# Kernel tuning notes

Measured on AMD Instinct MI355X. Metric: run time of the kernel, lower is better.

## Reference

```python
import jax, jax.numpy as jnp
import numpy as np

# dims
B, N, D, H, L = 2, 4096, 768, 12, 2
DH = D // H          # 64, equals BigBird block_size
BS = 64              # block size
NB = N // BS         # 64 blocks
R = 3                # num_random_blocks
FF = 4 * D
EPS = 1e-12          # BigBird layer_norm_eps


def _ln(x, g, b):
    mu = jnp.mean(x, -1, keepdims=True)
    var = jnp.mean(jnp.square(x - mu), -1, keepdims=True)
    return (x - mu) * jax.lax.rsqrt(var + EPS) * g + b


def _gelu_new(x):
    c = np.sqrt(2.0 / np.pi).astype(np.float32)
    return 0.5 * x * (1.0 + jnp.tanh(c * (x + 0.044715 * x * x * x)))


def _block_sparse_attn(q, k, v, rb):
    # q,k,v: [B,H,N,DH]; rb: [H,NB,R] random block ids (constant)
    scale = 1.0 / np.sqrt(DH).astype(np.float32)
    qb = q.reshape(B, H, NB, BS, DH)
    kb = k.reshape(B, H, NB, BS, DH)
    vb = v.reshape(B, H, NB, BS, DH)
    M = NB - 2
    mids = jnp.arange(1, NB - 1)
    win = jnp.stack([mids - 1, mids, mids + 1], -1)                    # [M,3]
    glb = jnp.broadcast_to(jnp.array([0, NB - 1], jnp.int32), (M, 2))  # [M,2]
    idx = jnp.concatenate([
        jnp.broadcast_to(glb[None], (H, M, 2)),
        jnp.broadcast_to(win[None], (H, M, 3)),
        rb[:, 1:NB - 1, :]], axis=-1)                                  # [H,M,8]
    hh = jnp.arange(H)[:, None, None]
    # gather key/value blocks: [B,H,M,8,BS,DH] -> [B,H,M,512,DH]
    kg = kb[:, hh, idx].reshape(B, H, M, -1, DH)
    vg = vb[:, hh, idx].reshape(B, H, M, -1, DH)
    qm = qb[:, :, 1:NB - 1]                                            # [B,H,M,BS,DH]
    s = jnp.einsum('bhmqd,bhmkd->bhmqk', qm, kg) * scale
    cm = jnp.einsum('bhmqk,bhmkd->bhmqd', jax.nn.softmax(s, -1), vg)
    # first and last query blocks attend globally (full attention)
    qe = jnp.stack([qb[:, :, 0], qb[:, :, -1]], 2)                     # [B,H,2,BS,DH]
    se = jnp.einsum('bheqd,bhkd->bheqk', qe, k) * scale
    ce = jnp.einsum('bheqk,bhkd->bheqd', jax.nn.softmax(se, -1), v)
    out = jnp.concatenate([ce[:, :, :1], cm, ce[:, :, 1:]], axis=2)    # [B,H,NB,BS,DH]
    return out.reshape(B, H, N, DH)


def _forward(inputs_embeds, rand_blocks, pos_emb, tt_emb, emb_ln_g, emb_ln_b,
             Wq, bq, Wk, bk, Wv, bv, Wo, bo, ln1_g, ln1_b,
             Wi, bi, Wd, bd, ln2_g, ln2_b, fc_w, fc_b):
    x = inputs_embeds + pos_emb[None] + tt_emb                         # embeddings (token_type id 0)
    x = _ln(x, emb_ln_g, emb_ln_b)
    for l in range(L):
        q = (x @ Wq[l] + bq[l]).reshape(B, N, H, DH).transpose(0, 2, 1, 3)
        k = (x @ Wk[l] + bk[l]).reshape(B, N, H, DH).transpose(0, 2, 1, 3)
        v = (x @ Wv[l] + bv[l]).reshape(B, N, H, DH).transpose(0, 2, 1, 3)
        ctx = _block_sparse_attn(q, k, v, rand_blocks[l])
        ctx = ctx.transpose(0, 2, 1, 3).reshape(B, N, D)
        a = _ln(x + ctx @ Wo[l] + bo[l], ln1_g[l], ln1_b[l])
        h = _gelu_new(a @ Wi[l] + bi[l])
        x = _ln(a + h @ Wd[l] + bd[l], ln2_g[l], ln2_b[l])
    pooled = jnp.mean(x, axis=1)                                       # [B,D]; dropout is identity at eval
    return (pooled @ fc_w + fc_b).squeeze()                            # [B]


def setup_inputs() -> dict:
    key = jax.random.key(0)
    ks = jax.random.split(key, 24)
    s = 0.02
    nrm = lambda k, shp: jax.random.normal(k, shp, jnp.float32) * s
    return {
        'inputs_embeds': jax.random.normal(ks[0], (B, N, D), jnp.float32),
        'rand_blocks': jax.random.randint(ks[1], (L, H, NB, R), 0, NB, jnp.int32),
        'pos_emb': nrm(ks[2], (N, D)),
        'tt_emb': nrm(ks[3], (D,)),
        'emb_ln_g': jnp.ones((D,), jnp.float32), 'emb_ln_b': jnp.zeros((D,), jnp.float32),
        'Wq': nrm(ks[4], (L, D, D)), 'bq': jnp.zeros((L, D), jnp.float32),
        'Wk': nrm(ks[5], (L, D, D)), 'bk': jnp.zeros((L, D), jnp.float32),
        'Wv': nrm(ks[6], (L, D, D)), 'bv': jnp.zeros((L, D), jnp.float32),
        'Wo': nrm(ks[7], (L, D, D)), 'bo': jnp.zeros((L, D), jnp.float32),
        'ln1_g': jnp.ones((L, D), jnp.float32), 'ln1_b': jnp.zeros((L, D), jnp.float32),
        'Wi': nrm(ks[8], (L, D, FF)), 'bi': jnp.zeros((L, FF), jnp.float32),
        'Wd': nrm(ks[9], (L, FF, D)), 'bd': jnp.zeros((L, D), jnp.float32),
        'ln2_g': jnp.ones((L, D), jnp.float32), 'ln2_b': jnp.zeros((L, D), jnp.float32),
        'fc_w': nrm(ks[10], (D, 1)), 'fc_b': jnp.zeros((1,), jnp.float32),
    }


def reference(inputs_embeds, rand_blocks, pos_emb, tt_emb, emb_ln_g, emb_ln_b,
              Wq, bq, Wk, bk, Wv, bv, Wo, bo, ln1_g, ln1_b,
              Wi, bi, Wd, bd, ln2_g, ln2_b, fc_w, fc_b):
    return _forward(inputs_embeds, rand_blocks, pos_emb, tt_emb, emb_ln_g, emb_ln_b,
                    Wq, bq, Wk, bk, Wv, bv, Wo, bo, ln1_g, ln1_b,
                    Wi, bi, Wd, bd, ln2_g, ln2_b, fc_w, fc_b)
```

## Files before the change

### kernel.cpp

```cpp
#include <hip/hip_runtime.h>
#include <math.h>

#define B_ 2
#define N_ 4096
#define D_ 768
#define H_ 12
#define DH_ 64
#define NB_ 64
#define FF_ 3072
#define LAYERS_ 2
#define ROWS_ (B_ * N_)

typedef __attribute__((ext_vector_type(8))) short s16x8;
typedef __attribute__((ext_vector_type(8))) unsigned short u16x8;
typedef __attribute__((ext_vector_type(4))) float f32x4;

typedef const __attribute__((address_space(1))) unsigned int ga_u32;
typedef __attribute__((address_space(3))) unsigned int lds_u32;

static __device__ __forceinline__ float gelu_fast(float x) {
    float z2 = 1.5957691216057308f * x * (1.0f + 0.044715f * x * x);
    return x * __builtin_amdgcn_rcpf(1.0f + __expf(-z2));
}

static __device__ __forceinline__ unsigned bf16_rne(float f) {
    unsigned u = __float_as_uint(f);
    return (u + 0x7FFFu + ((u >> 16) & 1u)) >> 16;
}
static __device__ __forceinline__ float bfh2f(unsigned short h) {
    return __uint_as_float(((unsigned)h) << 16);
}

__global__ __launch_bounds__(256)
void prep_weights(const float* __restrict__ Wq, const float* __restrict__ Wk,
                  const float* __restrict__ Wv, const float* __restrict__ Wo,
                  const float* __restrict__ Wi, const float* __restrict__ Wd,
                  unsigned short* __restrict__ Wt) {
    const size_t LW = 7077888;
    int bid = blockIdx.x;
    int l = bid / 1728, r = bid % 1728;
    const float* W; unsigned short* T; int K, N, t, nx;
    if (r < 576) {
        int which = r / 144; t = r % 144; nx = 12; K = 768; N = 768;
        W = (which == 0 ? Wq : which == 1 ? Wk : which == 2 ? Wv : Wo) + (size_t)l * D_ * D_;
        T = Wt + l * LW + (size_t)(which < 3 ? which * 768 * 768 : 2304 * 768);
    } else if (r < 1152) {
        t = r - 576; nx = 48; K = 768; N = 3072;
        W = Wi + (size_t)l * D_ * FF_;
        T = Wt + l * LW + (size_t)(2304 * 768 + 768 * 768);
    } else {
        t = r - 1152; nx = 12; K = 3072; N = 768;
        W = Wd + (size_t)l * FF_ * D_;
        T = Wt + l * LW + (size_t)(2304 * 768 + 768 * 768 + 3072 * 768);
    }
    const int bx = t % nx, by = t / nx;
    __shared__ unsigned short tile[64][72];
    const int k0 = by * 64, n0 = bx * 64;
    const int tt = threadIdx.x;
    const int rr = tt >> 2, c0 = (tt & 3) * 16;
    const float* src = W + (size_t)(k0 + rr) * N + n0 + c0;
#pragma unroll
    for (int j = 0; j < 4; ++j) {
        float4 v = *(const float4*)(src + j * 4);
        tile[rr][c0 + j * 4 + 0] = (unsigned short)bf16_rne(v.x);
        tile[rr][c0 + j * 4 + 1] = (unsigned short)bf16_rne(v.y);
        tile[rr][c0 + j * 4 + 2] = (unsigned short)bf16_rne(v.z);
        tile[rr][c0 + j * 4 + 3] = (unsigned short)bf16_rne(v.w);
    }
    __syncthreads();
    const int nr = tt >> 2, kc = (tt & 3) * 16;
    unsigned short* dst = T + (size_t)(n0 + nr) * K + k0 + kc;
    ushort4 o;
#pragma unroll
    for (int j = 0; j < 4; ++j) {
        o.x = tile[kc + j * 4 + 0][nr];
        o.y = tile[kc + j * 4 + 1][nr];
        o.z = tile[kc + j * 4 + 2][nr];
        o.w = tile[kc + j * 4 + 3][nr];
        *(ushort4*)(dst + j * 4) = o;
    }
}

template <int OMODE>
__global__ __launch_bounds__(256)
void gemm_bt(const unsigned short* __restrict__ A, const unsigned short* __restrict__ Bt,
             const float* __restrict__ bias, void* __restrict__ Cv,
             int N, int K, int gelu) {
    __shared__ __align__(16) unsigned short smem[2 * 8192];
    const int tid = threadIdx.x, lane = tid & 63, wid = tid >> 6;
    const int bid = blockIdx.x;
    const int row0 = (bid & 63) * 128, col0 = (bid >> 6) * 128;
    const int rh = (wid >> 1) * 64, ch = (wid & 1) * 64;
    const int fr = lane & 15, fq = lane >> 4;
    const int srow = wid * 32 + (lane >> 2);
    const int skoff = (lane & 3) * 8;
    const unsigned short* gA0 = A + (size_t)(row0 + srow) * K + skoff;
    const unsigned short* gA1 = gA0 + (size_t)16 * K;
    const unsigned short* gB0 = Bt + (size_t)(col0 + srow) * K + skoff;
    const unsigned short* gB1 = gB0 + (size_t)16 * K;

    f32x4 acc[4][4] = {};
    const int nk = K >> 5;
    {
        unsigned short* s = smem;
        __builtin_amdgcn_global_load_lds((ga_u32*)gA0, (lds_u32*)&s[wid * 1024], 16, 0, 0);
        __builtin_amdgcn_global_load_lds((ga_u32*)gA1, (lds_u32*)&s[wid * 1024 + 512], 16, 0, 0);
        __builtin_amdgcn_global_load_lds((ga_u32*)gB0, (lds_u32*)&s[4096 + wid * 1024], 16, 0, 0);
        __builtin_amdgcn_global_load_lds((ga_u32*)gB1, (lds_u32*)&s[4096 + wid * 1024 + 512], 16, 0, 0);
    }
    for (int kt = 0; kt < nk; ++kt) {
        __syncthreads();
        if (kt + 1 < nk) {
            int k0 = (kt + 1) << 5;
            unsigned short* s = smem + ((kt + 1) & 1) * 8192;
            __builtin_amdgcn_global_load_lds((ga_u32*)(gA0 + k0), (lds_u32*)&s[wid * 1024], 16, 0, 0);
            __builtin_amdgcn_global_load_lds((ga_u32*)(gA1 + k0), (lds_u32*)&s[wid * 1024 + 512], 16, 0, 0);
            __builtin_amdgcn_global_load_lds((ga_u32*)(gB0 + k0), (lds_u32*)&s[4096 + wid * 1024], 16, 0, 0);
            __builtin_amdgcn_global_load_lds((ga_u32*)(gB1 + k0), (lds_u32*)&s[4096 + wid * 1024 + 512], 16, 0, 0);
        }
        const unsigned short* sA = smem + (kt & 1) * 8192;
        const unsigned short* sB = sA + 4096;
        s16x8 af[4], bf[4];
#pragma unroll
        for (int i = 0; i < 4; ++i)
            af[i] = *(const s16x8*)&sA[(rh + 16 * i + fr) * 32 + fq * 8];
#pragma unroll
        for (int j = 0; j < 4; ++j)
            bf[j] = *(const s16x8*)&sB[(ch + 16 * j + fr) * 32 + fq * 8];
#pragma unroll
        for (int i = 0; i < 4; ++i)
#pragma unroll
            for (int j = 0; j < 4; ++j)
                acc[i][j] = __builtin_amdgcn_mfma_f32_16x16x32_bf16(af[i], bf[j], acc[i][j], 0, 0, 0);
    }
    if (OMODE == 0) {
#pragma unroll
        for (int j = 0; j < 4; ++j) {
            int col = col0 + ch + 16 * j + fr;
            float bb = bias[col];
#pragma unroll
            for (int i = 0; i < 4; ++i)
#pragma unroll
                for (int r = 0; r < 4; ++r) {
                    int row = row0 + rh + 16 * i + fq * 4 + r;
                    float v = acc[i][j][r] + bb;
                    if (gelu) v = gelu_fast(v);
                    ((float*)Cv)[(size_t)row * N + col] = v;
                }
        }
    } else {
        unsigned short* sC = smem;
#pragma unroll
        for (int hh = 0; hh < 2; ++hh) {
            __syncthreads();
            if ((wid >> 1) == hh) {
#pragma unroll
                for (int j = 0; j < 4; ++j) {
                    float bb = bias[col0 + ch + 16 * j + fr];
#pragma unroll
                    for (int i = 0; i < 4; ++i)
#pragma unroll
                        for (int r = 0; r < 4; ++r) {
                            float v = acc[i][j][r] + bb;
                            if (gelu) v = gelu_fast(v);
                            sC[(16 * i + fq * 4 + r) * 136 + ch + 16 * j + fr] =
                                (unsigned short)bf16_rne(v);
                        }
                }
            }
            __syncthreads();
#pragma unroll
            for (int p = 0; p < 4; ++p) {
                int seg = p * 256 + tid;
                int r = seg >> 4, c8 = (seg & 15) * 8;
                *(u16x8*)&((unsigned short*)Cv)[(size_t)(row0 + hh * 64 + r) * N + col0 + c8] =
                    *(const u16x8*)&sC[r * 136 + c8];
            }
        }
    }
}

__global__ __launch_bounds__(256)
void gemm_qkv(const unsigned short* __restrict__ A, const unsigned short* __restrict__ Bt,
              const float* __restrict__ bq, const float* __restrict__ bk,
              const float* __restrict__ bv,
              unsigned short* __restrict__ Qh, unsigned short* __restrict__ Kh,
              unsigned short* __restrict__ VT) {
    const int K = D_;
    __shared__ __align__(16) unsigned short smem[2 * 8192];
    const int tid = threadIdx.x, lane = tid & 63, wid = tid >> 6;
    const int bid = blockIdx.x;
    const int row0 = (bid & 63) * 128;
    const int bx = bid >> 6;
    const int col0 = bx * 128;
    const int rh = (wid >> 1) * 64, ch = (wid & 1) * 64;
    const int fr = lane & 15, fq = lane >> 4;
    const int srow = wid * 32 + (lane >> 2);
    const int skoff = (lane & 3) * 8;
    const unsigned short* gA0 = A + (size_t)(row0 + srow) * K + skoff;
    const unsigned short* gA1 = gA0 + (size_t)16 * K;
    const unsigned short* gB0 = Bt + (size_t)(col0 + srow) * K + skoff;
    const unsigned short* gB1 = gB0 + (size_t)16 * K;

    f32x4 acc[4][4] = {};
    const int nk = K >> 5;
    {
        unsigned short* s = smem;
        __builtin_amdgcn_global_load_lds((ga_u32*)gA0, (lds_u32*)&s[wid * 1024], 16, 0, 0);
        __builtin_amdgcn_global_load_lds((ga_u32*)gA1, (lds_u32*)&s[wid * 1024 + 512], 16, 0, 0);
        __builtin_amdgcn_global_load_lds((ga_u32*)gB0, (lds_u32*)&s[4096 + wid * 1024], 16, 0, 0);
        __builtin_amdgcn_global_load_lds((ga_u32*)gB1, (lds_u32*)&s[4096 + wid * 1024 + 512], 16, 0, 0);
    }
    for (int kt = 0; kt < nk; ++kt) {
        __syncthreads();
        if (kt + 1 < nk) {
            int k0 = (kt + 1) << 5;
            unsigned short* s = smem + ((kt + 1) & 1) * 8192;
            __builtin_amdgcn_global_load_lds((ga_u32*)(gA0 + k0), (lds_u32*)&s[wid * 1024], 16, 0, 0);
            __builtin_amdgcn_global_load_lds((ga_u32*)(gA1 + k0), (lds_u32*)&s[wid * 1024 + 512], 16, 0, 0);
            __builtin_amdgcn_global_load_lds((ga_u32*)(gB0 + k0), (lds_u32*)&s[4096 + wid * 1024], 16, 0, 0);
            __builtin_amdgcn_global_load_lds((ga_u32*)(gB1 + k0), (lds_u32*)&s[4096 + wid * 1024 + 512], 16, 0, 0);
        }
        const unsigned short* sA = smem + (kt & 1) * 8192;
        const unsigned short* sB = sA + 4096;
        s16x8 af[4], bf[4];
#pragma unroll
        for (int i = 0; i < 4; ++i)
            af[i] = *(const s16x8*)&sA[(rh + 16 * i + fr) * 32 + fq * 8];
#pragma unroll
        for (int j = 0; j < 4; ++j)
            bf[j] = *(const s16x8*)&sB[(ch + 16 * j + fr) * 32 + fq * 8];
#pragma unroll
        for (int i = 0; i < 4; ++i)
#pragma unroll
            for (int j = 0; j < 4; ++j)
                acc[i][j] = __builtin_amdgcn_mfma_f32_16x16x32_bf16(af[i], bf[j], acc[i][j], 0, 0, 0);
    }
    const int seg = bx / 6;
    const int colbase = col0 - seg * D_;
    const float* bias = (seg == 0) ? bq : (seg == 1) ? bk : bv;
    if (seg == 2) {
#pragma unroll
        for (int j = 0; j < 4; ++j) {
            int col_l = colbase + ch + 16 * j + fr;
            float bb = bias[col_l];
#pragma unroll
            for (int i = 0; i < 4; ++i) {
                int rowbase = row0 + rh + 16 * i + fq * 4;
                ushort4 o;
                o.x = (unsigned short)bf16_rne(acc[i][j][0] + bb);
                o.y = (unsigned short)bf16_rne(acc[i][j][1] + bb);
                o.z = (unsigned short)bf16_rne(acc[i][j][2] + bb);
                o.w = (unsigned short)bf16_rne(acc[i][j][3] + bb);
                *(ushort4*)&VT[(size_t)col_l * ROWS_ + rowbase] = o;
            }
        }
    } else {
        unsigned short* dst = (seg == 0) ? Qh : Kh;
        unsigned short* sC = smem;
#pragma unroll
        for (int hh = 0; hh < 2; ++hh) {
            __syncthreads();
            if ((wid >> 1) == hh) {
#pragma unroll
                for (int j = 0; j < 4; ++j) {
                    float bb = bias[colbase + ch + 16 * j + fr];
#pragma unroll
                    for (int i = 0; i < 4; ++i)
#pragma unroll
                        for (int r = 0; r < 4; ++r)
                            sC[(16 * i + fq * 4 + r) * 136 + ch + 16 * j + fr] =
                                (unsigned short)bf16_rne(acc[i][j][r] + bb);
                }
            }
            __syncthreads();
#pragma unroll
            for (int p = 0; p < 4; ++p) {
                int seg2 = p * 256 + tid;
                int r = seg2 >> 4, c8 = (seg2 & 15) * 8;
                *(u16x8*)&dst[(size_t)(row0 + hh * 64 + r) * D_ + colbase + c8] =
                    *(const u16x8*)&sC[r * 136 + c8];
            }
        }
    }
}

template <bool EDGE>
__global__ __launch_bounds__(256, 4)
void attn_mfma(const unsigned short* __restrict__ Qb, const unsigned short* __restrict__ Kb,
               const unsigned short* __restrict__ VTb, const int* __restrict__ rb,
               unsigned short* __restrict__ ctx, float* __restrict__ scratch) {
    __shared__ __align__(16) unsigned short sQ[64][72];
    __shared__ __align__(16) unsigned short sK[64][72];
    __shared__ __align__(16) unsigned short sVT[64][72];
    __shared__ __align__(16) unsigned short sP[4][16][72];
    __shared__ int sList[16];
    const int tid = threadIdx.x, lane = tid & 63, wid = tid >> 6;
    const int fr = lane & 15, fq = lane >> 4;
    int qb, h, b, nkb, slice = 0;
    if (EDGE) {
        int part = blockIdx.x & 3;
        int hh = (blockIdx.x >> 2) % H_;
        int be = (blockIdx.x >> 2) / H_;
        int eb = be & 1;
        b = be >> 1;
        h = hh;
        qb = eb ? (NB_ - 1) : 0;
        nkb = 16;
        slice = ((b * 2 + eb) * H_ + h) * 4 + part;
        if (tid < 16) sList[tid] = part * 16 + tid;
    } else {
        qb = blockIdx.x % (NB_ - 2) + 1;
        h = (blockIdx.x / (NB_ - 2)) % H_;
        b = blockIdx.x / ((NB_ - 2) * H_);
        nkb = 8;
        if (tid < 8) {
            int e;
            if (tid == 0) e = 0;
            else if (tid == 1) e = NB_ - 1;
            else if (tid < 5) e = qb + (tid - 3);
            else e = rb[(h * NB_ + qb) * 3 + (tid - 5)];
            sList[tid] = e;
        }
    }
    const int qrow0 = b * N_ + qb * 64;
    const unsigned short* Qg = Qb + (size_t)qrow0 * D_ + h * 64;
#pragma unroll
    for (int p = 0; p < 2; ++p) {
        int idx = p * 256 + tid;
        int r = idx >> 3, o = (idx & 7) * 8;
        *(u16x8*)&sQ[r][o] = *(const u16x8*)(Qg + (size_t)r * D_ + o);
    }
    f32x4 oacc[4] = {};
    float l_part[4] = {};
    __syncthreads();
    s16x8 aq0 = *(const s16x8*)&sQ[wid * 16 + fr][fq * 8];
    s16x8 aq1 = *(const s16x8*)&sQ[wid * 16 + fr][32 + fq * 8];

    const int stg_r = tid >> 3, stg_o = (tid & 7) * 8;
    u16x8 kreg[2], vreg[2];
    {
        int keyrow0 = b * N_ + sList[0] * 64;
        const unsigned short* Kg = Kb + (size_t)keyrow0 * D_ + h * 64;
        const unsigned short* Vg = VTb + (size_t)(h * 64) * ROWS_ + keyrow0;
#pragma unroll
        for (int p = 0; p < 2; ++p) {
            int r = stg_r + p * 32;
            kreg[p] = *(const u16x8*)(Kg + (size_t)r * D_ + stg_o);
            vreg[p] = *(const u16x8*)(Vg + (size_t)r * ROWS_ + stg_o);
        }
    }

    for (int kb = 0; kb < nkb; ++kb) {
        __syncthreads();
#pragma unroll
        for (int p = 0; p < 2; ++p) {
            int r = stg_r + p * 32;
            *(u16x8*)&sK[r][stg_o] = kreg[p];
            *(u16x8*)&sVT[r][stg_o] = vreg[p];
        }
        __syncthreads();
        if (kb + 1 < nkb) {
            int keyrow0 = b * N_ + sList[kb + 1] * 64;
            const unsigned short* Kg = Kb + (size_t)keyrow0 * D_ + h * 64;
            const unsigned short* Vg = VTb + (size_t)(h * 64) * ROWS_ + keyrow0;
#pragma unroll
            for (int p = 0; p < 2; ++p) {
                int r = stg_r + p * 32;
                kreg[p] = *(const u16x8*)(Kg + (size_t)r * D_ + stg_o);
                vreg[p] = *(const u16x8*)(Vg + (size_t)r * ROWS_ + stg_o);
            }
        }
#pragma unroll
        for (int g = 0; g < 4; ++g) {
            s16x8 bk0 = *(const s16x8*)&sK[g * 16 + fr][fq * 8];
            s16x8 bk1 = *(const s16x8*)&sK[g * 16 + fr][32 + fq * 8];
            f32x4 s = {};
            s = __builtin_amdgcn_mfma_f32_16x16x32_bf16(aq0, bk0, s, 0, 0, 0);
            s = __builtin_amdgcn_mfma_f32_16x16x32_bf16(aq1, bk1, s, 0, 0, 0);
#pragma unroll
            for (int r = 0; r < 4; ++r) {
                float pv = __expf(s[r] * 0.125f);
                l_part[r] += pv;
                sP[wid][fq * 4 + r][g * 16 + fr] = (unsigned short)bf16_rne(pv);
            }
        }
        s16x8 ap0 = *(const s16x8*)&sP[wid][fr][fq * 8];
        s16x8 ap1 = *(const s16x8*)&sP[wid][fr][32 + fq * 8];
#pragma unroll
        for (int g = 0; g < 4; ++g) {
            s16x8 bv0 = *(const s16x8*)&sVT[g * 16 + fr][fq * 8];
            s16x8 bv1 = *(const s16x8*)&sVT[g * 16 + fr][32 + fq * 8];
            oacc[g] = __builtin_amdgcn_mfma_f32_16x16x32_bf16(ap0, bv0, oacc[g], 0, 0, 0);
            oacc[g] = __builtin_amdgcn_mfma_f32_16x16x32_bf16(ap1, bv1, oacc[g], 0, 0, 0);
        }
    }
    float l4[4];
#pragma unroll
    for (int r = 0; r < 4; ++r) {
        float lv = l_part[r];
        lv += __shfl_xor(lv, 1, 64);
        lv += __shfl_xor(lv, 2, 64);
        lv += __shfl_xor(lv, 4, 64);
        lv += __shfl_xor(lv, 8, 64);
        l4[r] = lv;
    }
    if (EDGE) {
        float* sc = scratch + (size_t)slice * (64 * 64 + 64);
#pragma unroll
        for (int g = 0; g < 4; ++g)
#pragma unroll
            for (int r = 0; r < 4; ++r)
                sc[(wid * 16 + fq * 4 + r) * 64 + g * 16 + fr] = oacc[g][r];
        if (fr == 0) {
#pragma unroll
            for (int r = 0; r < 4; ++r)
                sc[4096 + wid * 16 + fq * 4 + r] = l4[r];
        }
    } else {
        __syncthreads();
#pragma unroll
        for (int g = 0; g < 4; ++g) {
#pragma unroll
            for (int r = 0; r < 4; ++r) {
                float v = oacc[g][r] / l4[r];
                sK[wid * 16 + fq * 4 + r][g * 16 + fr] = (unsigned short)bf16_rne(v);
            }
        }
        __syncthreads();
        unsigned short* Cg = ctx + (size_t)qrow0 * D_ + h * 64;
#pragma unroll
        for (int p = 0; p < 2; ++p) {
            int idx = p * 256 + tid;
            int r = idx >> 3, o = (idx & 7) * 8;
            *(u16x8*)(Cg + (size_t)r * D_ + o) = *(const u16x8*)&sK[r][o];
        }
    }
}

__global__ __launch_bounds__(256)
void edge_combine(const float* __restrict__ scratch, unsigned short* __restrict__ ctx) {
    const int bid = blockIdx.x;
    const int h = bid % H_;
    const int eb = (bid / H_) & 1;
    const int b = bid / (2 * H_);
    const int qb = eb ? (NB_ - 1) : 0;
    const int qrow0 = b * N_ + qb * 64;
    const int slice0 = bid * 4;
    for (int e = threadIdx.x; e < 4096; e += 256) {
        int row = e >> 6, col = e & 63;
        float o = 0.f, l = 0.f;
#pragma unroll
        for (int p = 0; p < 4; ++p) {
            const float* sc = scratch + (size_t)(slice0 + p) * (64 * 64 + 64);
            o += sc[row * 64 + col];
            l += sc[4096 + row];
        }
        ctx[(size_t)(qrow0 + row) * D_ + h * 64 + col] = (unsigned short)bf16_rne(o / l);
    }
}

__global__ __launch_bounds__(256)
void embed_ln_kernel(const float* __restrict__ emb, const float* __restrict__ pos,
                     const float* __restrict__ tt, const float* __restrict__ g,
                     const float* __restrict__ bb, unsigned short* __restrict__ out) {
    __shared__ float red1[4], red2[4];
    const int row = blockIdx.x;
    const int n = row & (N_ - 1);
    const int t = threadIdx.x;
    float v[3];
#pragma unroll
    for (int i = 0; i < 3; ++i) {
        int d = t + i * 256;
        v[i] = emb[(size_t)row * D_ + d] + pos[(size_t)n * D_ + d] + tt[d];
    }
    float s = v[0] + v[1] + v[2];
#pragma unroll
    for (int off = 32; off > 0; off >>= 1) s += __shfl_xor(s, off, 64);
    if ((t & 63) == 0) red1[t >> 6] = s;
    __syncthreads();
    float mu = (red1[0] + red1[1] + red1[2] + red1[3]) * (1.0f / D_);
    float q = 0;
#pragma unroll
    for (int i = 0; i < 3; ++i) { float dv = v[i] - mu; q += dv * dv; }
#pragma unroll
    for (int off = 32; off > 0; off >>= 1) q += __shfl_xor(q, off, 64);
    if ((t & 63) == 0) red2[t >> 6] = q;
    __syncthreads();
    float var = (red2[0] + red2[1] + red2[2] + red2[3]) * (1.0f / D_);
    float rs = rsqrtf(var + 1e-12f);
#pragma unroll
    for (int i = 0; i < 3; ++i) {
        int d = t + i * 256;
        out[(size_t)row * D_ + d] = (unsigned short)bf16_rne((v[i] - mu) * rs * g[d] + bb[d]);
    }
}

__global__ __launch_bounds__(256)
void add_ln_kernel(const unsigned short* __restrict__ X, const unsigned short* __restrict__ Y,
                   const float* __restrict__ g, const float* __restrict__ bb,
                   unsigned short* __restrict__ out) {
    __shared__ float red1[4], red2[4];
    const int row = blockIdx.x;
    const int t = threadIdx.x;
    float v[3];
#pragma unroll
    for (int i = 0; i < 3; ++i) {
        int d = t + i * 256;
        v[i] = bfh2f(X[(size_t)row * D_ + d]) + bfh2f(Y[(size_t)row * D_ + d]);
    }
    float s = v[0] + v[1] + v[2];
#pragma unroll
    for (int off = 32; off > 0; off >>= 1) s += __shfl_xor(s, off, 64);
    if ((t & 63) == 0) red1[t >> 6] = s;
    __syncthreads();
    float mu = (red1[0] + red1[1] + red1[2] + red1[3]) * (1.0f / D_);
    float q = 0;
#pragma unroll
    for (int i = 0; i < 3; ++i) { float dv = v[i] - mu; q += dv * dv; }
#pragma unroll
    for (int off = 32; off > 0; off >>= 1) q += __shfl_xor(q, off, 64);
    if ((t & 63) == 0) red2[t >> 6] = q;
    __syncthreads();
    float var = (red2[0] + red2[1] + red2[2] + red2[3]) * (1.0f / D_);
    float rs = rsqrtf(var + 1e-12f);
#pragma unroll
    for (int i = 0; i < 3; ++i) {
        int d = t + i * 256;
        out[(size_t)row * D_ + d] = (unsigned short)bf16_rne((v[i] - mu) * rs * g[d] + bb[d]);
    }
}

__global__ __launch_bounds__(256)
void pool_partial_kernel(const unsigned short* __restrict__ X, float* __restrict__ partial) {
    int blk = blockIdx.x;
    int b = blk >> 4, c = blk & 15;
    int t = threadIdx.x;
#pragma unroll
    for (int i = 0; i < 3; ++i) {
        int d = t + i * 256;
        float s = 0.f;
        for (int n = 0; n < 256; ++n)
            s += bfh2f(X[((size_t)(b * N_ + c * 256 + n)) * D_ + d]);
        partial[(size_t)(b * 16 + c) * D_ + d] = s;
    }
}

__global__ __launch_bounds__(256)
void pool_final_kernel(const float* __restrict__ partial, const float* __restrict__ fcw,
                       const float* __restrict__ fcb, float* __restrict__ out) {
    __shared__ float red[4];
    int t = threadIdx.x;
    for (int b = 0; b < B_; ++b) {
        float s = 0.f;
#pragma unroll
        for (int i = 0; i < 3; ++i) {
            int d = t + i * 256;
            float ps = 0.f;
#pragma unroll
            for (int c = 0; c < 16; ++c) ps += partial[(size_t)(b * 16 + c) * D_ + d];
            s += ps * (1.0f / N_) * fcw[d];
        }
#pragma unroll
        for (int off = 32; off > 0; off >>= 1) s += __shfl_xor(s, off, 64);
        __syncthreads();
        if ((t & 63) == 0) red[t >> 6] = s;
        __syncthreads();
        if (t == 0) out[b] = red[0] + red[1] + red[2] + red[3] + fcb[0];
    }
}

extern "C" void kernel_launch(void* const* d_in, const int* in_sizes, int n_in,
                              void* d_out, int out_size, void* d_ws, size_t ws_size,
                              hipStream_t stream) {
    (void)in_sizes; (void)n_in; (void)out_size; (void)ws_size;
    const float* emb  = (const float*)d_in[0];
    const int*   rblk = (const int*)d_in[1];
    const float* pos  = (const float*)d_in[2];
    const float* tt   = (const float*)d_in[3];
    const float* elg  = (const float*)d_in[4];
    const float* elb  = (const float*)d_in[5];
    const float* Wq   = (const float*)d_in[6];
    const float* bq   = (const float*)d_in[7];
    const float* Wk   = (const float*)d_in[8];
    const float* bk   = (const float*)d_in[9];
    const float* Wv   = (const float*)d_in[10];
    const float* bv   = (const float*)d_in[11];
    const float* Wo   = (const float*)d_in[12];
    const float* bo   = (const float*)d_in[13];
    const float* ln1g = (const float*)d_in[14];
    const float* ln1b = (const float*)d_in[15];
    const float* Wi   = (const float*)d_in[16];
    const float* bi   = (const float*)d_in[17];
    const float* Wd   = (const float*)d_in[18];
    const float* bd   = (const float*)d_in[19];
    const float* ln2g = (const float*)d_in[20];
    const float* ln2b = (const float*)d_in[21];
    const float* fcw  = (const float*)d_in[22];
    const float* fcb  = (const float*)d_in[23];
    float* outp = (float*)d_out;

    const size_t R = (size_t)ROWS_ * D_;
    float* base = (float*)d_ws;
    unsigned short* Xh  = (unsigned short*)base;
    unsigned short* Abh = (unsigned short*)(base + R / 2);
    unsigned short* Ob  = (unsigned short*)(base + R);
    unsigned short* Qh  = (unsigned short*)(base + 2 * R);
    unsigned short* Kh  = (unsigned short*)(base + 2 * R + R / 2);
    unsigned short* VTh = (unsigned short*)(base + 3 * R);
    unsigned short* Ch  = (unsigned short*)(base + 3 * R + R / 2);
    unsigned short* Hh  = (unsigned short*)(base + 2 * R);
    unsigned short* Wt  = (unsigned short*)(base + 4 * R);
    float* Esc = base + 4 * R + 7077888;
    float* Pp  = Esc + 798720;

    const size_t LW = 7077888;
    const int rows = ROWS_;
    dim3 blk(256);

    prep_weights<<<2 * 1728, blk, 0, stream>>>(Wq, Wk, Wv, Wo, Wi, Wd, Wt);

    embed_ln_kernel<<<rows, blk, 0, stream>>>(emb, pos, tt, elg, elb, Xh);

    for (int l = 0; l < LAYERS_; ++l) {
        const float* bq_l = bq + (size_t)l * D_;
        const float* bk_l = bk + (size_t)l * D_;
        const float* bv_l = bv + (size_t)l * D_;
        const float* bo_l = bo + (size_t)l * D_;
        const float* bi_l = bi + (size_t)l * FF_;
        const float* bd_l = bd + (size_t)l * D_;
        const float* l1g = ln1g + (size_t)l * D_;
        const float* l1b = ln1b + (size_t)l * D_;
        const float* l2g = ln2g + (size_t)l * D_;
        const float* l2b = ln2b + (size_t)l * D_;
        const int* rb_l = rblk + (size_t)l * H_ * NB_ * 3;
        unsigned short* QKVt = Wt + l * LW;
        unsigned short* Ot = QKVt + 2304 * 768;
        unsigned short* It = Ot + 768 * 768;
        unsigned short* Dt = It + 3072 * 768;

        gemm_qkv<<<18 * 64, blk, 0, stream>>>(Xh, QKVt, bq_l, bk_l, bv_l, Qh, Kh, VTh);

        attn_mfma<false><<<B_ * H_ * (NB_ - 2), blk, 0, stream>>>(Qh, Kh, VTh, rb_l, Ch, Esc);
        attn_mfma<true><<<B_ * 2 * H_ * 4, blk, 0, stream>>>(Qh, Kh, VTh, rb_l, Ch, Esc);
        edge_combine<<<B_ * 2 * H_, blk, 0, stream>>>(Esc, Ch);

        gemm_bt<1><<<6 * 64, blk, 0, stream>>>(Ch, Ot, bo_l, Ob, D_, D_, 0);
        add_ln_kernel<<<rows, blk, 0, stream>>>(Xh, Ob, l1g, l1b, Abh);

        gemm_bt<1><<<24 * 64, blk, 0, stream>>>(Abh, It, bi_l, Hh, FF_, D_, 1);
        gemm_bt<1><<<6 * 64, blk, 0, stream>>>(Hh, Dt, bd_l, Ob, D_, FF_, 0);

        add_ln_kernel<<<rows, blk, 0, stream>>>(Abh, Ob, l2g, l2b, Xh);
    }

    pool_partial_kernel<<<B_ * 16, blk, 0, stream>>>(Xh, Pp);
    pool_final_kernel<<<1, blk, 0, stream>>>(Pp, fcw, fcb, outp);
}
```

Baseline: 747.7 us.

## Use 256x128 GEMM tiles for QKV/FFN-up and split-K for FFN-down

Adds 256x128-tile GEMM kernels (8x4 MFMA accumulators per wave, two blocks per CU) for the QKV projection and the FFN up-projection, which halves the number of blocks and raises operand reuse per LDS load. The FFN down-projection (K=3072, only 384 tiles) is split into two K halves via blockIdx.y, each writing bf16 partial sums, and a new add_ln2 kernel sums the residual with both partials before the layer norm. This targets CU under-utilisation on the narrow down-projection GEMM. The cost is extra partial-sum traffic, a bf16 rounding of each partial, and higher register pressure in the larger tiles.

```diff
diff --git a/kernel.cpp b/kernel.cpp
--- a/kernel.cpp
+++ b/kernel.cpp
@@ -81,26 +81,240 @@
     }
 }
 
-template <int OMODE>
+__global__ __launch_bounds__(256, 2)
+void gemm_bt256(const unsigned short* __restrict__ A, const unsigned short* __restrict__ Bt,
+                const float* __restrict__ bias, unsigned short* __restrict__ Cv,
+                int N, int K, int gelu) {
+    __shared__ __align__(16) unsigned short smem[2 * 12288];
+    const int tid = threadIdx.x, lane = tid & 63, wid = tid >> 6;
+    const int bid = blockIdx.x;
+    const int row0 = (bid & 31) * 256, col0 = (bid >> 5) * 128;
+    const int wh = wid >> 1, wc = wid & 1;
+    const int fr = lane & 15, fq = lane >> 4;
+    const int slr = lane >> 2, slo = (lane & 3) * 8;
+
+    const unsigned short* gA[4];
+    const unsigned short* gB[2];
+#pragma unroll
+    for (int c = 0; c < 4; ++c)
+        gA[c] = A + (size_t)(row0 + wid * 64 + c * 16 + slr) * K + slo;
+#pragma unroll
+    for (int c = 0; c < 2; ++c)
+        gB[c] = Bt + (size_t)(col0 + wid * 32 + c * 16 + slr) * K + slo;
+
+    f32x4 acc[8][4] = {};
+    const int nk = K >> 5;
+    {
+        unsigned short* s = smem;
+#pragma unroll
+        for (int c = 0; c < 4; ++c)
+            __builtin_amdgcn_global_load_lds((ga_u32*)gA[c],
+                (lds_u32*)&s[(wid * 64 + c * 16) * 32], 16, 0, 0);
+#pragma unroll
+        for (int c = 0; c < 2; ++c)
+            __builtin_amdgcn_global_load_lds((ga_u32*)gB[c],
+                (lds_u32*)&s[8192 + (wid * 32 + c * 16) * 32], 16, 0, 0);
+    }
+    for (int kt = 0; kt < nk; ++kt) {
+        __syncthreads();
+        if (kt + 1 < nk) {
+            int k0 = (kt + 1) << 5;
+            unsigned short* s = smem + ((kt + 1) & 1) * 12288;
+#pragma unroll
+            for (int c = 0; c < 4; ++c)
+                __builtin_amdgcn_global_load_lds((ga_u32*)(gA[c] + k0),
+                    (lds_u32*)&s[(wid * 64 + c * 16) * 32], 16, 0, 0);
+#pragma unroll
+            for (int c = 0; c < 2; ++c)
+                __builtin_amdgcn_global_load_lds((ga_u32*)(gB[c] + k0),
+                    (lds_u32*)&s[8192 + (wid * 32 + c * 16) * 32], 16, 0, 0);
+        }
+        const unsigned short* sA = smem + (kt & 1) * 12288;
+        const unsigned short* sB = sA + 8192;
+        s16x8 af[8], bf[4];
+#pragma unroll
+        for (int i = 0; i < 8; ++i)
+            af[i] = *(const s16x8*)&sA[(wh * 128 + 16 * i + fr) * 32 + fq * 8];
+#pragma unroll
+        for (int j = 0; j < 4; ++j)
+            bf[j] = *(const s16x8*)&sB[(wc * 64 + 16 * j + fr) * 32 + fq * 8];
+#pragma unroll
+        for (int i = 0; i < 8; ++i)
+#pragma unroll
+            for (int j = 0; j < 4; ++j)
+                acc[i][j] = __builtin_amdgcn_mfma_f32_16x16x32_bf16(af[i], bf[j], acc[i][j], 0, 0, 0);
+    }
+    unsigned short* sC = smem;
+#pragma unroll
+    for (int hh = 0; hh < 4; ++hh) {
+        __syncthreads();
+        if (wh == (hh >> 1)) {
+#pragma unroll
+            for (int j = 0; j < 4; ++j) {
+                float bb = bias[col0 + wc * 64 + 16 * j + fr];
+#pragma unroll
+                for (int i2 = 0; i2 < 4; ++i2) {
+                    int i = (hh & 1) * 4 + i2;
+#pragma unroll
+                    for (int r = 0; r < 4; ++r) {
+                        float v = acc[i][j][r] + bb;
+                        if (gelu) v = gelu_fast(v);
+                        sC[(16 * i2 + fq * 4 + r) * 136 + wc * 64 + 16 * j + fr] =
+                            (unsigned short)bf16_rne(v);
+                    }
+                }
+            }
+        }
+        __syncthreads();
+#pragma unroll
+        for (int p = 0; p < 4; ++p) {
+            int seg = p * 256 + tid;
+            int r = seg >> 4, c8 = (seg & 15) * 8;
+            *(u16x8*)&Cv[(size_t)(row0 + hh * 64 + r) * N + col0 + c8] =
+                *(const u16x8*)&sC[r * 136 + c8];
+        }
+    }
+}
+
+__global__ __launch_bounds__(256, 2)
+void gemm_qkv256(const unsigned short* __restrict__ A, const unsigned short* __restrict__ Bt,
+                 const float* __restrict__ bq, const float* __restrict__ bk,
+                 const float* __restrict__ bv,
+                 unsigned short* __restrict__ Qh, unsigned short* __restrict__ Kh,
+                 unsigned short* __restrict__ VT) {
+    const int K = D_;
+    __shared__ __align__(16) unsigned short smem[2 * 12288];
+    const int tid = threadIdx.x, lane = tid & 63, wid = tid >> 6;
+    const int bid = blockIdx.x;
+    const int row0 = (bid & 31) * 256;
+    const int bx = bid >> 5;
+    const int col0 = bx * 128;
+    const int wh = wid >> 1, wc = wid & 1;
+    const int fr = lane & 15, fq = lane >> 4;
+    const int slr = lane >> 2, slo = (lane & 3) * 8;
+
+    const unsigned short* gA[4];
+    const unsigned short* gB[2];
+#pragma unroll
+    for (int c = 0; c < 4; ++c)
+        gA[c] = A + (size_t)(row0 + wid * 64 + c * 16 + slr) * K + slo;
+#pragma unroll
+    for (int c = 0; c < 2; ++c)
+        gB[c] = Bt + (size_t)(col0 + wid * 32 + c * 16 + slr) * K + slo;
+
+    f32x4 acc[8][4] = {};
+    const int nk = K >> 5;
+    {
+        unsigned short* s = smem;
+#pragma unroll
+        for (int c = 0; c < 4; ++c)
+            __builtin_amdgcn_global_load_lds((ga_u32*)gA[c],
+                (lds_u32*)&s[(wid * 64 + c * 16) * 32], 16, 0, 0);
+#pragma unroll
+        for (int c = 0; c < 2; ++c)
+            __builtin_amdgcn_global_load_lds((ga_u32*)gB[c],
+                (lds_u32*)&s[8192 + (wid * 32 + c * 16) * 32], 16, 0, 0);
+    }
+    for (int kt = 0; kt < nk; ++kt) {
+        __syncthreads();
+        if (kt + 1 < nk) {
+            int k0 = (kt + 1) << 5;
+            unsigned short* s = smem + ((kt + 1) & 1) * 12288;
+#pragma unroll
+            for (int c = 0; c < 4; ++c)
+                __builtin_amdgcn_global_load_lds((ga_u32*)(gA[c] + k0),
+                    (lds_u32*)&s[(wid * 64 + c * 16) * 32], 16, 0, 0);
+#pragma unroll
+            for (int c = 0; c < 2; ++c)
+                __builtin_amdgcn_global_load_lds((ga_u32*)(gB[c] + k0),
+                    (lds_u32*)&s[8192 + (wid * 32 + c * 16) * 32], 16, 0, 0);
+        }
+        const unsigned short* sA = smem + (kt & 1) * 12288;
+        const unsigned short* sB = sA + 8192;
+        s16x8 af[8], bf[4];
+#pragma unroll
+        for (int i = 0; i < 8; ++i)
+            af[i] = *(const s16x8*)&sA[(wh * 128 + 16 * i + fr) * 32 + fq * 8];
+#pragma unroll
+        for (int j = 0; j < 4; ++j)
+            bf[j] = *(const s16x8*)&sB[(wc * 64 + 16 * j + fr) * 32 + fq * 8];
+#pragma unroll
+        for (int i = 0; i < 8; ++i)
+#pragma unroll
+            for (int j = 0; j < 4; ++j)
+                acc[i][j] = __builtin_amdgcn_mfma_f32_16x16x32_bf16(af[i], bf[j], acc[i][j], 0, 0, 0);
+    }
+    const int seg = bx / 6;
+    const int colbase = col0 - seg * D_;
+    const float* bias = (seg == 0) ? bq : (seg == 1) ? bk : bv;
+    if (seg == 2) {
+#pragma unroll
+        for (int j = 0; j < 4; ++j) {
+            int col_l = colbase + wc * 64 + 16 * j + fr;
+            float bb = bias[col_l];
+#pragma unroll
+            for (int i = 0; i < 8; ++i) {
+                int rowbase = row0 + wh * 128 + 16 * i + fq * 4;
+                ushort4 o;
+                o.x = (unsigned short)bf16_rne(acc[i][j][0] + bb);
+                o.y = (unsigned short)bf16_rne(acc[i][j][1] + bb);
+                o.z = (unsigned short)bf16_rne(acc[i][j][2] + bb);
+                o.w = (unsigned short)bf16_rne(acc[i][j][3] + bb);
+                *(ushort4*)&VT[(size_t)col_l * ROWS_ + rowbase] = o;
+            }
+        }
+    } else {
+        unsigned short* dst = (seg == 0) ? Qh : Kh;
+        unsigned short* sC = smem;
+#pragma unroll
+        for (int hh = 0; hh < 4; ++hh) {
+            __syncthreads();
+            if (wh == (hh >> 1)) {
+#pragma unroll
+                for (int j = 0; j < 4; ++j) {
+                    float bb = bias[colbase + wc * 64 + 16 * j + fr];
+#pragma unroll
+                    for (int i2 = 0; i2 < 4; ++i2) {
+                        int i = (hh & 1) * 4 + i2;
+#pragma unroll
+                        for (int r = 0; r < 4; ++r)
+                            sC[(16 * i2 + fq * 4 + r) * 136 + wc * 64 + 16 * j + fr] =
+                                (unsigned short)bf16_rne(acc[i][j][r] + bb);
+                    }
+                }
+            }
+            __syncthreads();
+#pragma unroll
+            for (int p = 0; p < 4; ++p) {
+                int seg2 = p * 256 + tid;
+                int r = seg2 >> 4, c8 = (seg2 & 15) * 8;
+                *(u16x8*)&dst[(size_t)(row0 + hh * 64 + r) * D_ + colbase + c8] =
+                    *(const u16x8*)&sC[r * 136 + c8];
+            }
+        }
+    }
+}
+
 __global__ __launch_bounds__(256)
 void gemm_bt(const unsigned short* __restrict__ A, const unsigned short* __restrict__ Bt,
-             const float* __restrict__ bias, void* __restrict__ Cv,
-             int N, int K, int gelu) {
+             const float* __restrict__ bias, unsigned short* __restrict__ Cv,
+             int N, int K, int klen) {
     __shared__ __align__(16) unsigned short smem[2 * 8192];
     const int tid = threadIdx.x, lane = tid & 63, wid = tid >> 6;
-    const int bid = blockIdx.x;
+    const int bid = blockIdx.x, part = blockIdx.y;
+    const int kbeg = part * klen;
     const int row0 = (bid & 63) * 128, col0 = (bid >> 6) * 128;
     const int rh = (wid >> 1) * 64, ch = (wid & 1) * 64;
     const int fr = lane & 15, fq = lane >> 4;
     const int srow = wid * 32 + (lane >> 2);
     const int skoff = (lane & 3) * 8;
-    const unsigned short* gA0 = A + (size_t)(row0 + srow) * K + skoff;
+    const unsigned short* gA0 = A + (size_t)(row0 + srow) * K + kbeg + skoff;
     const unsigned short* gA1 = gA0 + (size_t)16 * K;
-    const unsigned short* gB0 = Bt + (size_t)(col0 + srow) * K + skoff;
+    const unsigned short* gB0 = Bt + (size_t)(col0 + srow) * K + kbeg + skoff;
     const unsigned short* gB1 = gB0 + (size_t)16 * K;
 
     f32x4 acc[4][4] = {};
-    const int nk = K >> 5;
+    const int nk = klen >> 5;
     {
         unsigned short* s = smem;
         __builtin_amdgcn_global_load_lds((ga_u32*)gA0, (lds_u32*)&s[wid * 1024], 16, 0, 0);
@@ -133,154 +347,32 @@
             for (int j = 0; j < 4; ++j)
                 acc[i][j] = __builtin_amdgcn_mfma_f32_16x16x32_bf16(af[i], bf[j], acc[i][j], 0, 0, 0);
     }
-    if (OMODE == 0) {
-#pragma unroll
-        for (int j = 0; j < 4; ++j) {
-            int col = col0 + ch + 16 * j + fr;
-            float bb = bias[col];
-#pragma unroll
-            for (int i = 0; i < 4; ++i)
-#pragma unroll
-                for (int r = 0; r < 4; ++r) {
-                    int row = row0 + rh + 16 * i + fq * 4 + r;
-                    float v = acc[i][j][r] + bb;
-                    if (gelu) v = gelu_fast(v);
-                    ((float*)Cv)[(size_t)row * N + col] = v;
-                }
-        }
-    } else {
-        unsigned short* sC = smem;
-#pragma unroll
-        for (int hh = 0; hh < 2; ++hh) {
-            __syncthreads();
-            if ((wid >> 1) == hh) {
-#pragma unroll
-                for (int j = 0; j < 4; ++j) {
-                    float bb = bias[col0 + ch + 16 * j + fr];
-#pragma unroll
-                    for (int i = 0; i < 4; ++i)
-#pragma unroll
-                        for (int r = 0; r < 4; ++r) {
-                            float v = acc[i][j][r] + bb;
-                            if (gelu) v = gelu_fast(v);
-                            sC[(16 * i + fq * 4 + r) * 136 + ch + 16 * j + fr] =
-                                (unsigned short)bf16_rne(v);
-                        }
-                }
+    unsigned short* out = Cv + (size_t)part * ROWS_ * N;
+    unsigned short* sC = smem;
+#pragma unroll
+    for (int hh = 0; hh < 2; ++hh) {
+        __syncthreads();
+        if ((wid >> 1) == hh) {
+#pragma unroll
+            for (int j = 0; j < 4; ++j) {
+                float bb = (part == 0) ? bias[col0 + ch + 16 * j + fr] : 0.0f;
+#pragma unroll
+                for (int i = 0; i < 4; ++i)
+#pragma unroll
+                    for (int r = 0; r < 4; ++r) {
+                        float v = acc[i][j][r] + bb;
+                        sC[(16 * i + fq * 4 + r) * 136 + ch + 16 * j + fr] =
+                            (unsigned short)bf16_rne(v);
+                    }
             }
-            __syncthreads();
-#pragma unroll
-            for (int p = 0; p < 4; ++p) {
-                int seg = p * 256 + tid;
-                int r = seg >> 4, c8 = (seg & 15) * 8;
-                *(u16x8*)&((unsigned short*)Cv)[(size_t)(row0 + hh * 64 + r) * N + col0 + c8] =
-                    *(const u16x8*)&sC[r * 136 + c8];
-            }
-        }
-    }
-}
-
-__global__ __launch_bounds__(256)
-void gemm_qkv(const unsigned short* __restrict__ A, const unsigned short* __restrict__ Bt,
-              const float* __restrict__ bq, const float* __restrict__ bk,
-              const float* __restrict__ bv,
-              unsigned short* __restrict__ Qh, unsigned short* __restrict__ Kh,
-              unsigned short* __restrict__ VT) {
-    const int K = D_;
-    __shared__ __align__(16) unsigned short smem[2 * 8192];
-    const int tid = threadIdx.x, lane = tid & 63, wid = tid >> 6;
-    const int bid = blockIdx.x;
-    const int row0 = (bid & 63) * 128;
-    const int bx = bid >> 6;
-    const int col0 = bx * 128;
-    const int rh = (wid >> 1) * 64, ch = (wid & 1) * 64;
-    const int fr = lane & 15, fq = lane >> 4;
-    const int srow = wid * 32 + (lane >> 2);
-    const int skoff = (lane & 3) * 8;
-    const unsigned short* gA0 = A + (size_t)(row0 + srow) * K + skoff;
-    const unsigned short* gA1 = gA0 + (size_t)16 * K;
-    const unsigned short* gB0 = Bt + (size_t)(col0 + srow) * K + skoff;
-    const unsigned short* gB1 = gB0 + (size_t)16 * K;
-
-    f32x4 acc[4][4] = {};
-    const int nk = K >> 5;
-    {
-        unsigned short* s = smem;
-        __builtin_amdgcn_global_load_lds((ga_u32*)gA0, (lds_u32*)&s[wid * 1024], 16, 0, 0);
-        __builtin_amdgcn_global_load_lds((ga_u32*)gA1, (lds_u32*)&s[wid * 1024 + 512], 16, 0, 0);
-        __builtin_amdgcn_global_load_lds((ga_u32*)gB0, (lds_u32*)&s[4096 + wid * 1024], 16, 0, 0);
-        __builtin_amdgcn_global_load_lds((ga_u32*)gB1, (lds_u32*)&s[4096 + wid * 1024 + 512], 16, 0, 0);
-    }
-    for (int kt = 0; kt < nk; ++kt) {
-        __syncthreads();
-        if (kt + 1 < nk) {
-            int k0 = (kt + 1) << 5;
-            unsigned short* s = smem + ((kt + 1) & 1) * 8192;
-            __builtin_amdgcn_global_load_lds((ga_u32*)(gA0 + k0), (lds_u32*)&s[wid * 1024], 16, 0, 0);
-            __builtin_amdgcn_global_load_lds((ga_u32*)(gA1 + k0), (lds_u32*)&s[wid * 1024 + 512], 16, 0, 0);
-            __builtin_amdgcn_global_load_lds((ga_u32*)(gB0 + k0), (lds_u32*)&s[4096 + wid * 1024], 16, 0, 0);
-            __builtin_amdgcn_global_load_lds((ga_u32*)(gB1 + k0), (lds_u32*)&s[4096 + wid * 1024 + 512], 16, 0, 0);
-        }
-        const unsigned short* sA = smem + (kt & 1) * 8192;
-        const unsigned short* sB = sA + 4096;
-        s16x8 af[4], bf[4];
-#pragma unroll
-        for (int i = 0; i < 4; ++i)
-            af[i] = *(const s16x8*)&sA[(rh + 16 * i + fr) * 32 + fq * 8];
-#pragma unroll
-        for (int j = 0; j < 4; ++j)
-            bf[j] = *(const s16x8*)&sB[(ch + 16 * j + fr) * 32 + fq * 8];
-#pragma unroll
-        for (int i = 0; i < 4; ++i)
-#pragma unroll
-            for (int j = 0; j < 4; ++j)
-                acc[i][j] = __builtin_amdgcn_mfma_f32_16x16x32_bf16(af[i], bf[j], acc[i][j], 0, 0, 0);
-    }
-    const int seg = bx / 6;
-    const int colbase = col0 - seg * D_;
-    const float* bias = (seg == 0) ? bq : (seg == 1) ? bk : bv;
-    if (seg == 2) {
-#pragma unroll
-        for (int j = 0; j < 4; ++j) {
-            int col_l = colbase + ch + 16 * j + fr;
-            float bb = bias[col_l];
-#pragma unroll
-            for (int i = 0; i < 4; ++i) {
-                int rowbase = row0 + rh + 16 * i + fq * 4;
-                ushort4 o;
-                o.x = (unsigned short)bf16_rne(acc[i][j][0] + bb);
-                o.y = (unsigned short)bf16_rne(acc[i][j][1] + bb);
-                o.z = (unsigned short)bf16_rne(acc[i][j][2] + bb);
-                o.w = (unsigned short)bf16_rne(acc[i][j][3] + bb);
-                *(ushort4*)&VT[(size_t)col_l * ROWS_ + rowbase] = o;
-            }
-        }
-    } else {
-        unsigned short* dst = (seg == 0) ? Qh : Kh;
-        unsigned short* sC = smem;
-#pragma unroll
-        for (int hh = 0; hh < 2; ++hh) {
-            __syncthreads();
-            if ((wid >> 1) == hh) {
-#pragma unroll
-                for (int j = 0; j < 4; ++j) {
-                    float bb = bias[colbase + ch + 16 * j + fr];
-#pragma unroll
-                    for (int i = 0; i < 4; ++i)
-#pragma unroll
-                        for (int r = 0; r < 4; ++r)
-                            sC[(16 * i + fq * 4 + r) * 136 + ch + 16 * j + fr] =
-                                (unsigned short)bf16_rne(acc[i][j][r] + bb);
-                }
-            }
-            __syncthreads();
-#pragma unroll
-            for (int p = 0; p < 4; ++p) {
-                int seg2 = p * 256 + tid;
-                int r = seg2 >> 4, c8 = (seg2 & 15) * 8;
-                *(u16x8*)&dst[(size_t)(row0 + hh * 64 + r) * D_ + colbase + c8] =
-                    *(const u16x8*)&sC[r * 136 + c8];
-            }
+        }
+        __syncthreads();
+#pragma unroll
+        for (int p = 0; p < 4; ++p) {
+            int seg = p * 256 + tid;
+            int r = seg >> 4, c8 = (seg & 15) * 8;
+            *(u16x8*)&out[(size_t)(row0 + hh * 64 + r) * N + col0 + c8] =
+                *(const u16x8*)&sC[r * 136 + c8];
         }
     }
 }
@@ -532,6 +624,43 @@
 }
 
 __global__ __launch_bounds__(256)
+void add_ln2_kernel(const unsigned short* __restrict__ X, const unsigned short* __restrict__ Y0,
+                    const unsigned short* __restrict__ Y1,
+                    const float* __restrict__ g, const float* __restrict__ bb,
+                    unsigned short* __restrict__ out) {
+    __shared__ float red1[4], red2[4];
+    const int row = blockIdx.x;
+    const int t = threadIdx.x;
+    float v[3];
+#pragma unroll
+    for (int i = 0; i < 3; ++i) {
+        int d = t + i * 256;
+        size_t o = (size_t)row * D_ + d;
+        v[i] = bfh2f(X[o]) + bfh2f(Y0[o]) + bfh2f(Y1[o]);
+    }
+    float s = v[0] + v[1] + v[2];
+#pragma unroll
+    for (int off = 32; off > 0; off >>= 1) s += __shfl_xor(s, off, 64);
+    if ((t & 63) == 0) red1[t >> 6] = s;
+    __syncthreads();
+    float mu = (red1[0] + red1[1] + red1[2] + red1[3]) * (1.0f / D_);
+    float q = 0;
+#pragma unroll
+    for (int i = 0; i < 3; ++i) { float dv = v[i] - mu; q += dv * dv; }
+#pragma unroll
+    for (int off = 32; off > 0; off >>= 1) q += __shfl_xor(q, off, 64);
+    if ((t & 63) == 0) red2[t >> 6] = q;
+    __syncthreads();
+    float var = (red2[0] + red2[1] + red2[2] + red2[3]) * (1.0f / D_);
+    float rs = rsqrtf(var + 1e-12f);
+#pragma unroll
+    for (int i = 0; i < 3; ++i) {
+        int d = t + i * 256;
+        out[(size_t)row * D_ + d] = (unsigned short)bf16_rne((v[i] - mu) * rs * g[d] + bb[d]);
+    }
+}
+
+__global__ __launch_bounds__(256)
 void pool_partial_kernel(const unsigned short* __restrict__ X, float* __restrict__ partial) {
     int blk = blockIdx.x;
     int b = blk >> 4, c = blk & 15;
@@ -610,6 +739,7 @@
     unsigned short* VTh = (unsigned short*)(base + 3 * R);
     unsigned short* Ch  = (unsigned short*)(base + 3 * R + R / 2);
     unsigned short* Hh  = (unsigned short*)(base + 2 * R);
+    unsigned short* Yp  = (unsigned short*)(base + 3 * R);
     unsigned short* Wt  = (unsigned short*)(base + 4 * R);
     float* Esc = base + 4 * R + 7077888;
     float* Pp  = Esc + 798720;
@@ -639,19 +769,19 @@
         unsigned short* It = Ot + 768 * 768;
         unsigned short* Dt = It + 3072 * 768;
 
-        gemm_qkv<<<18 * 64, blk, 0, stream>>>(Xh, QKVt, bq_l, bk_l, bv_l, Qh, Kh, VTh);
+        gemm_qkv256<<<18 * 32, blk, 0, stream>>>(Xh, QKVt, bq_l, bk_l, bv_l, Qh, Kh, VTh);
 
         attn_mfma<false><<<B_ * H_ * (NB_ - 2), blk, 0, stream>>>(Qh, Kh, VTh, rb_l, Ch, Esc);
         attn_mfma<true><<<B_ * 2 * H_ * 4, blk, 0, stream>>>(Qh, Kh, VTh, rb_l, Ch, Esc);
         edge_combine<<<B_ * 2 * H_, blk, 0, stream>>>(Esc, Ch);
 
-        gemm_bt<1><<<6 * 64, blk, 0, stream>>>(Ch, Ot, bo_l, Ob, D_, D_, 0);
+        gemm_bt<<<dim3(6 * 64, 1), blk, 0, stream>>>(Ch, Ot, bo_l, Ob, D_, D_, D_);
         add_ln_kernel<<<rows, blk, 0, stream>>>(Xh, Ob, l1g, l1b, Abh);
 
-        gemm_bt<1><<<24 * 64, blk, 0, stream>>>(Abh, It, bi_l, Hh, FF_, D_, 1);
-        gemm_bt<1><<<6 * 64, blk, 0, stream>>>(Hh, Dt, bd_l, Ob, D_, FF_, 0);
-
-        add_ln_kernel<<<rows, blk, 0, stream>>>(Abh, Ob, l2g, l2b, Xh);
+        gemm_bt256<<<24 * 32, blk, 0, stream>>>(Abh, It, bi_l, Hh, FF_, D_, 1);
+        gemm_bt<<<dim3(6 * 64, 2), blk, 0, stream>>>(Hh, Dt, bd_l, Yp, D_, FF_, FF_ / 2);
+
+        add_ln2_kernel<<<rows, blk, 0, stream>>>(Abh, Yp, Yp + R, l2g, l2b, Xh);
     }
 
     pool_partial_kernel<<<B_ * 16, blk, 0, stream>>>(Xh, Pp);
```

Result: slower. 791.1 us (+5.8%).
